# Optimization experiments

Hardware: AMD Instinct MI355X
Metric: run time of the kernel (lower is better)

Reference implementation:

```python
import jax, jax.numpy as jnp
import numpy as np
import math

D_MODEL = 1024
NUM_HEADS = 16
HEAD_DIM = D_MODEL // NUM_HEADS
CLAMP = 1e9


def setup_inputs() -> dict:
    key = jax.random.key(0)
    k1, k2, k3, k4, k5 = jax.random.split(key, 5)
    B, S = 2, 2048
    x = jax.random.normal(k1, (B, S, D_MODEL), dtype=jnp.float32)
    # torch Linear params, stored as [in, out] (y = x @ W + b)
    s1 = 1.0 / math.sqrt(D_MODEL)
    W_qkv = jax.random.uniform(k2, (D_MODEL, 3 * D_MODEL), jnp.float32, -s1, s1)
    b_qkv = jax.random.uniform(k3, (3 * D_MODEL,), jnp.float32, -s1, s1)
    W_out = jax.random.uniform(k4, (D_MODEL, D_MODEL), jnp.float32, -s1, s1)
    b_out = jax.random.uniform(k5, (D_MODEL,), jnp.float32, -s1, s1)
    return {"x": x, "W_qkv": W_qkv, "b_qkv": b_qkv, "W_out": W_out, "b_out": b_out}


def reference(x, W_qkv, b_qkv, W_out, b_out):
    B, S, D = x.shape
    qkv = x @ W_qkv + b_qkv                       # [B, S, 3*D]
    qkv = qkv.reshape(B, S, NUM_HEADS, 3 * HEAD_DIM).transpose(0, 2, 1, 3)  # [B, H, S, 3*hd]
    q, k, v = jnp.split(qkv, 3, axis=-1)          # each [B, H, S, hd]
    scale = 1.0 / math.sqrt(HEAD_DIM)
    scores = jnp.einsum('bhqd,bhkd->bhqk', q, k) * scale  # [B, H, S, S]
    causal = jnp.tril(jnp.ones((S, S), dtype=bool))
    scores = jnp.where(causal, scores, -jnp.inf)
    scores = jnp.clip(scores, -CLAMP, CLAMP)      # -inf -> -1e9, matching torch clamp
    attn = jax.nn.softmax(scores, axis=-1)
    values = jnp.einsum('bhqk,bhkd->bhqd', attn, v)        # [B, H, S, hd]
    values = values.transpose(0, 2, 1, 3).reshape(B, S, D)  # [B, S, D]
    out = values @ W_out + b_out
    # dropout is identity in eval mode
    return out
```

## Files before the change

kernel.cpp:

```cpp
#include <hip/hip_runtime.h>
#include <hip/hip_bf16.h>

#define D_MODEL 1024
#define NUM_HEADS 16
#define HEAD_DIM 64
#define SEQ 2048
#define BATCH 2
#define ROWS (BATCH * SEQ)

typedef unsigned short u16;
typedef __bf16 bf16x8 __attribute__((ext_vector_type(8)));
typedef float f32x4 __attribute__((ext_vector_type(4)));

__device__ inline u16 f2bfu(float f) {
  unsigned u = __float_as_uint(f);
  unsigned r = (u + 0x7fffu + ((u >> 16) & 1u)) >> 16;
  return (u16)r;
}

__device__ inline unsigned cvt_pk_bf16(float a, float b) {
#if __has_builtin(__builtin_amdgcn_cvt_pk_bf16_f32)
  auto r = __builtin_amdgcn_cvt_pk_bf16_f32(a, b);
  unsigned u;
  __builtin_memcpy(&u, &r, 4);
  return u;
#else
  return (unsigned)f2bfu(a) | ((unsigned)f2bfu(b) << 16);
#endif
}

__device__ inline f32x4 mfma16(bf16x8 a, bf16x8 b, f32x4 c) {
  return __builtin_amdgcn_mfma_f32_16x16x32_bf16(a, b, c, 0, 0, 0);
}

__device__ inline bf16x8 load_frag(const u16* p) {
  union { uint4 v; bf16x8 f; } u;
  u.v = *(const uint4*)p;
  return u.f;
}

__device__ inline void gload_lds16(const u16* g, u16* l) {
  __builtin_amdgcn_global_load_lds((const __attribute__((address_space(1))) void*)g,
                                   (__attribute__((address_space(3))) void*)l, 16, 0, 0);
}


__global__ __launch_bounds__(256) void prep_kernel(const float* __restrict__ x,
                                                   u16* __restrict__ xb,
                                                   const float* __restrict__ Wq,
                                                   u16* __restrict__ WqT,
                                                   const float* __restrict__ Wo,
                                                   u16* __restrict__ WoT) {
  __shared__ float t[32][33];
  const int bid = blockIdx.x;
  if (bid < 4096) {
    int i = bid * 256 + threadIdx.x;
    float4 v = ((const float4*)x)[i];
    uint2 o;
    o.x = cvt_pk_bf16(v.x, v.y);
    o.y = cvt_pk_bf16(v.z, v.w);
    ((uint2*)xb)[i] = o;
    return;
  }
  const float* W;
  u16* Wt;
  int N, tIdx;
  if (bid < 4096 + 3072) { W = Wq; Wt = WqT; N = 3072; tIdx = bid - 4096; }
  else                   { W = Wo; Wt = WoT; N = 1024; tIdx = bid - 7168; }
  const int k0 = (tIdx & 31) * 32, n0 = (tIdx >> 5) * 32;
  const int c = threadIdx.x & 31, r8 = threadIdx.x >> 5;
#pragma unroll
  for (int i = 0; i < 4; i++) {
    int r = r8 + i * 8;
    t[r][c] = W[(size_t)(k0 + r) * N + n0 + c];
  }
  __syncthreads();
#pragma unroll
  for (int i = 0; i < 4; i++) {
    int r = r8 + i * 8;
    Wt[(size_t)(n0 + r) * 1024 + k0 + c] = f2bfu(t[c][r]);
  }
}


__global__ __launch_bounds__(256, 3) void gemm_qkv(const u16* __restrict__ A,
                                                   const u16* __restrict__ Bt,
                                                   const float* __restrict__ bias,
                                                   u16* __restrict__ Qb, u16* __restrict__ Kb,
                                                   u16* __restrict__ Vt) {
  __shared__ u16 lA[3][128 * 32], lB[3][128 * 32];
  const int tid = threadIdx.x;
  const int wave = tid >> 6, lane = tid & 63, ln = lane & 15, quad = lane >> 4;
  const int lin = blockIdx.y * 24 + blockIdx.x;
  const int reg = lin & 7, idx = lin >> 3;
  const int mr = idx / 12, nr = idx - mr * 12;
  const int m0 = ((reg >> 1) * 8 + mr) * 128;
  const int n0 = (((reg & 1) * 12) + nr) * 128;
  const int wm = (wave & 1) * 64, wn = (wave >> 1) * 64;
  f32x4 acc[4][4] = {};

  auto issue = [&](u16* dA, u16* dB, int k0) {
#pragma unroll
    for (int i = 0; i < 2; ++i) {
      int rb = wave * 2 + i;
      gload_lds16(A + (size_t)(m0 + rb * 16 + ln) * 1024 + k0 + quad * 8, dA + rb * 512);
      gload_lds16(Bt + (size_t)(n0 + rb * 16 + ln) * 1024 + k0 + quad * 8, dB + rb * 512);
    }
  };
  auto compute = [&](const u16* sA, const u16* sB) {
    bf16x8 a[4], b[4];
#pragma unroll
    for (int i = 0; i < 4; ++i) {
      a[i] = load_frag(sA + (wm / 16 + i) * 512 + quad * 128 + ln * 8);
      b[i] = load_frag(sB + (wn / 16 + i) * 512 + quad * 128 + ln * 8);
    }
#pragma unroll
    for (int mt = 0; mt < 4; ++mt)
#pragma unroll
      for (int nt = 0; nt < 4; ++nt) acc[mt][nt] = mfma16(a[mt], b[nt], acc[mt][nt]);
  };

  issue(lA[0], lB[0], 0);
  issue(lA[1], lB[1], 32);
  asm volatile("s_waitcnt vmcnt(4)" ::: "memory");
  asm volatile("s_barrier" ::: "memory");

  for (int tt = 0; tt < 10; ++tt) {
    const int t = tt * 3;
    issue(lA[2], lB[2], (t + 2) * 32);
    compute(lA[0], lB[0]);
    asm volatile("s_waitcnt vmcnt(4)" ::: "memory");
    asm volatile("s_barrier" ::: "memory");
    issue(lA[0], lB[0], (t + 3) * 32);
    compute(lA[1], lB[1]);
    asm volatile("s_waitcnt vmcnt(4)" ::: "memory");
    asm volatile("s_barrier" ::: "memory");
    issue(lA[1], lB[1], (t + 4) * 32);
    compute(lA[2], lB[2]);
    asm volatile("s_waitcnt vmcnt(4)" ::: "memory");
    asm volatile("s_barrier" ::: "memory");
  }
  compute(lA[0], lB[0]);
  asm volatile("s_waitcnt vmcnt(0)" ::: "memory");
  asm volatile("s_barrier" ::: "memory");
  compute(lA[1], lB[1]);

#pragma unroll
  for (int mt = 0; mt < 4; ++mt) {
    int row = m0 + wm + mt * 16 + quad * 4;
    int bb = row >> 11, s0 = row & 2047;
#pragma unroll
    for (int nt = 0; nt < 4; ++nt) {
      int col = n0 + wn + nt * 16 + ln;
      float bv = bias[col];
      int h = col / 192, rem = col - h * 192, t3 = rem >> 6, d = rem & 63;
      int bh = bb * NUM_HEADS + h;
      if (t3 == 2) {
        uint2 pk;
        pk.x = cvt_pk_bf16(acc[mt][nt][0] + bv, acc[mt][nt][1] + bv);
        pk.y = cvt_pk_bf16(acc[mt][nt][2] + bv, acc[mt][nt][3] + bv);
        *(uint2*)(Vt + ((size_t)bh * 64 + d) * SEQ + s0) = pk;
      } else {
        u16* dst = (t3 == 0) ? Qb : Kb;
#pragma unroll
        for (int r = 0; r < 4; ++r)
          dst[((size_t)bh * SEQ + s0 + r) * 64 + d] = f2bfu(acc[mt][nt][r] + bv);
      }
    }
  }
}


__global__ __launch_bounds__(512) void attn_kernel(const u16* __restrict__ Qb,
                                                   const u16* __restrict__ Kb,
                                                   const u16* __restrict__ Vt,
                                                   u16* __restrict__ Ob) {
  __shared__ u16 lK[2 * 2 * 64 * 64];
  __shared__ u16 lV[2 * 64 * 64];
  __shared__ u16 lP[8][1152];
  const int tid = threadIdx.x;
  const int wave = tid >> 6, lane = tid & 63;
  const int ln = lane & 15, quad = lane >> 4;
  const int lin = blockIdx.y * 16 + blockIdx.x;
  const int xreg = lin & 7, xidx = lin >> 3;
  const int j = xidx & 15;
  const int bh = xreg * 4 + (xidx >> 4);
  const int lo = j, hi = 31 - j;
  const int myt = (wave < 4) ? lo : hi;
  const int q0w = myt * 64 + (wave & 3) * 16;
  const int sD = myt >> 1;
  const int nsup = (hi + 2) >> 1;
  const u16* Qg = Qb + (size_t)bh * SEQ * 64;
  const u16* Kg = Kb + (size_t)bh * SEQ * 64;
  const u16* Vg = Vt + (size_t)bh * 64 * SEQ;
  u16* lPw = lP[wave];

  bf16x8 qf[2];
#pragma unroll
  for (int ks = 0; ks < 2; ++ks)
    qf[ks] = load_frag(Qg + (size_t)(q0w + ln) * 64 + ks * 32 + quad * 8);

  const u16* sp[4];
  u16* dp[4];
#pragma unroll
  for (int i = 0; i < 4; ++i) {
    if (wave < 4) {
      int c = wave * 4 + i, half = c >> 3, cc = c & 7, rb = cc >> 1, kgh = cc & 1;
      sp[i] = Kg + (size_t)(half * 64 + rb * 16 + ln) * 64 + (kgh * 4 + quad) * 8;
      dp[i] = lK + half * 4096 + rb * 1024 + kgh * 512;
    } else {
      int c2 = wave * 4 - 16 + i, half = c2 >> 3, cc = c2 & 7, rb = cc >> 1, kgh = cc & 1;
      sp[i] = Vg + (size_t)(rb * 16 + ln) * SEQ + half * 64 + (kgh * 4 + quad) * 8;
      dp[i] = lV + half * 4096 + rb * 1024 + kgh * 512;
    }
  }
  if (wave < 4) {
#pragma unroll
    for (int i = 0; i < 4; ++i) gload_lds16(sp[i], dp[i]);
  }

  f32x4 o[4] = {};
  float m_r = -1e30f;
  float l_r = 0.f;
  const float SC = 0.18033688011112042f;
  const int qq = q0w + ln;

  for (int s = 0; s < nsup; ++s) {
    __syncthreads();
    if (wave >= 4) {
#pragma unroll
      for (int i = 0; i < 4; ++i) gload_lds16(sp[i] + (size_t)s * 128, dp[i]);
    }

    if (s <= sD) {
      const u16* lKs = lK + (s & 1) * 8192;
      f32x4 sc[2][4] = {};
#pragma unroll
      for (int h = 0; h < 2; ++h)
#pragma unroll
        for (int mt = 0; mt < 4; ++mt)
#pragma unroll
          for (int ks = 0; ks < 2; ++ks) {
            bf16x8 kf = load_frag(lKs + h * 4096 + mt * 1024 + (ks * 4 + quad) * 128 + ln * 8);
            sc[h][mt] = mfma16(kf, qf[ks], sc[h][mt]);
          }
      if (s == sD) {
#pragma unroll
        for (int h = 0; h < 2; ++h)
#pragma unroll
          for (int mt = 0; mt < 4; ++mt) {
            int key0 = (2 * s + h) * 64 + mt * 16 + quad * 4;
#pragma unroll
            for (int r = 0; r < 4; ++r)
              if (key0 + r > qq) sc[h][mt][r] = -1e30f;
          }
      }
      float mloc = sc[0][0][0];
#pragma unroll
      for (int h = 0; h < 2; ++h)
#pragma unroll
        for (int mt = 0; mt < 4; ++mt)
#pragma unroll
          for (int r = 0; r < 4; ++r) mloc = fmaxf(mloc, sc[h][mt][r]);
      mloc = fmaxf(mloc, __shfl_xor(mloc, 16));
      mloc = fmaxf(mloc, __shfl_xor(mloc, 32));
      float mnew = fmaxf(m_r, mloc);
      float alpha = __builtin_amdgcn_exp2f((m_r - mnew) * SC);
      float nmsc = -mnew * SC;
      float sum = 0.f;
#pragma unroll
      for (int h = 0; h < 2; ++h)
#pragma unroll
        for (int mt = 0; mt < 4; ++mt)
#pragma unroll
          for (int r = 0; r < 4; ++r) {
            float p = __builtin_amdgcn_exp2f(__builtin_fmaf(sc[h][mt][r], SC, nmsc));
            sc[h][mt][r] = p;
            sum += p;
          }
      sum += __shfl_xor(sum, 16);
      sum += __shfl_xor(sum, 32);
      l_r = l_r * alpha + sum;
      m_r = mnew;
#pragma unroll
      for (int dt = 0; dt < 4; ++dt) o[dt] *= alpha;

      __syncthreads();
      if (wave < 4 && s + 1 < nsup) {
        u16* dsl = (u16*)((s + 1) & 1 ? 8192 : 0);
#pragma unroll
        for (int i = 0; i < 4; ++i)
          gload_lds16(sp[i] + (size_t)(s + 1) * (128 * 64), dp[i] + ((s + 1) & 1) * 8192);
        (void)dsl;
      }

#pragma unroll
      for (int h = 0; h < 2; ++h) {
#pragma unroll
        for (int mt = 0; mt < 4; ++mt) {
          uint2 pk;
          pk.x = cvt_pk_bf16(sc[h][mt][0], sc[h][mt][1]);
          pk.y = cvt_pk_bf16(sc[h][mt][2], sc[h][mt][3]);
          int addr = ln * 64 + (((mt * 2 + (quad >> 1)) ^ (ln & 7)) * 8) + (quad & 1) * 4;
          *(uint2*)(lPw + addr) = pk;
        }
        bf16x8 pf[2];
#pragma unroll
        for (int ks = 0; ks < 2; ++ks)
          pf[ks] = load_frag(lPw + ln * 64 + (((ks * 4 + quad) ^ (ln & 7)) * 8));
#pragma unroll
        for (int dt = 0; dt < 4; ++dt)
#pragma unroll
          for (int ks = 0; ks < 2; ++ks) {
            bf16x8 av = load_frag(lV + h * 4096 + dt * 1024 + (ks * 4 + quad) * 128 + ln * 8);
            o[dt] = mfma16(av, pf[ks], o[dt]);
          }
      }
    } else {
      __syncthreads();
      if (wave < 4 && s + 1 < nsup) {
#pragma unroll
        for (int i = 0; i < 4; ++i)
          gload_lds16(sp[i] + (size_t)(s + 1) * (128 * 64), dp[i] + ((s + 1) & 1) * 8192);
      }
    }
  }

  float inv = 1.f / l_r;
#pragma unroll
  for (int dt = 0; dt < 4; ++dt) {
    uint2 pk;
    pk.x = cvt_pk_bf16(o[dt][0] * inv, o[dt][1] * inv);
    pk.y = cvt_pk_bf16(o[dt][2] * inv, o[dt][3] * inv);
    *(uint2*)(lPw + ln * 72 + dt * 16 + quad * 4) = pk;
  }
  const int b = bh >> 4, h2 = bh & 15;
#pragma unroll
  for (int i = 0; i < 2; ++i) {
    int c = lane + i * 64;
    int qq2 = c >> 3, dg = c & 7;
    uint4 val = *(const uint4*)(lPw + qq2 * 72 + dg * 8);
    *(uint4*)(Ob + ((size_t)b * SEQ + q0w + qq2) * 1024 + h2 * 64 + dg * 8) = val;
  }
}


__global__ __launch_bounds__(256, 3) void gemm_out(const u16* __restrict__ A,
                                                   const u16* __restrict__ Bt,
                                                   const float* __restrict__ bias,
                                                   float* __restrict__ out) {
  __shared__ u16 lA[3][128 * 32], lB[3][64 * 32];
  const int tid = threadIdx.x;
  const int wave = tid >> 6, lane = tid & 63, ln = lane & 15, quad = lane >> 4;
  const int lin = blockIdx.y * 16 + blockIdx.x;
  const int reg = lin & 7, idx = lin >> 3;
  const int mr = idx >> 3, nr = idx & 7;
  const int m0 = ((reg >> 1) * 8 + mr) * 128;
  const int n0 = (((reg & 1) * 8) + nr) * 64;
  f32x4 acc[2][4] = {};

  auto issue = [&](u16* dA, u16* dB, int k0) {
#pragma unroll
    for (int i = 0; i < 3; ++i) {
      int c = wave * 3 + i;
      if (c < 8) {
        gload_lds16(A + (size_t)(m0 + c * 16 + ln) * 1024 + k0 + quad * 8, dA + c * 512);
      } else {
        int cc = c - 8;
        gload_lds16(Bt + (size_t)(n0 + cc * 16 + ln) * 1024 + k0 + quad * 8, dB + cc * 512);
      }
    }
  };
  auto compute = [&](const u16* sA, const u16* sB) {
    bf16x8 a[2], b[4];
#pragma unroll
    for (int i = 0; i < 2; ++i)
      a[i] = load_frag(sA + (wave * 2 + i) * 512 + quad * 128 + ln * 8);
#pragma unroll
    for (int i = 0; i < 4; ++i)
      b[i] = load_frag(sB + i * 512 + quad * 128 + ln * 8);
#pragma unroll
    for (int mt = 0; mt < 2; ++mt)
#pragma unroll
      for (int nt = 0; nt < 4; ++nt) acc[mt][nt] = mfma16(a[mt], b[nt], acc[mt][nt]);
  };

  issue(lA[0], lB[0], 0);
  issue(lA[1], lB[1], 32);
  asm volatile("s_waitcnt vmcnt(3)" ::: "memory");
  asm volatile("s_barrier" ::: "memory");

  for (int tt = 0; tt < 10; ++tt) {
    const int t = tt * 3;
    issue(lA[2], lB[2], (t + 2) * 32);
    compute(lA[0], lB[0]);
    asm volatile("s_waitcnt vmcnt(3)" ::: "memory");
    asm volatile("s_barrier" ::: "memory");
    issue(lA[0], lB[0], (t + 3) * 32);
    compute(lA[1], lB[1]);
    asm volatile("s_waitcnt vmcnt(3)" ::: "memory");
    asm volatile("s_barrier" ::: "memory");
    issue(lA[1], lB[1], (t + 4) * 32);
    compute(lA[2], lB[2]);
    asm volatile("s_waitcnt vmcnt(3)" ::: "memory");
    asm volatile("s_barrier" ::: "memory");
  }
  compute(lA[0], lB[0]);
  asm volatile("s_waitcnt vmcnt(0)" ::: "memory");
  asm volatile("s_barrier" ::: "memory");
  compute(lA[1], lB[1]);

#pragma unroll
  for (int mt = 0; mt < 2; ++mt) {
    int row = m0 + wave * 32 + mt * 16 + quad * 4;
#pragma unroll
    for (int nt = 0; nt < 4; ++nt) {
      int col = n0 + nt * 16 + ln;
      float bv = bias[col];
#pragma unroll
      for (int r = 0; r < 4; ++r)
        out[(size_t)(row + r) * 1024 + col] = acc[mt][nt][r] + bv;
    }
  }
}


extern "C" void kernel_launch(void* const* d_in, const int* in_sizes, int n_in,
                              void* d_out, int out_size, void* d_ws, size_t ws_size,
                              hipStream_t stream) {
  const float* x = (const float*)d_in[0];
  const float* W_qkv = (const float*)d_in[1];
  const float* b_qkv = (const float*)d_in[2];
  const float* W_out = (const float*)d_in[3];
  const float* b_out = (const float*)d_in[4];
  float* out = (float*)d_out;

  char* ws = (char*)d_ws;
  const size_t SZ_XB = (size_t)ROWS * D_MODEL * 2;
  const size_t SZ_WQKVT = (size_t)3 * D_MODEL * D_MODEL * 2;
  const size_t SZ_WOUTT = (size_t)D_MODEL * D_MODEL * 2;
  const size_t SZ_HEADS = (size_t)BATCH * NUM_HEADS * SEQ * HEAD_DIM * 2;
  u16* xb = (u16*)(ws);
  u16* WqkvT = (u16*)(ws + SZ_XB);
  u16* WoutT = (u16*)(ws + SZ_XB + SZ_WQKVT);
  u16* Qb = (u16*)(ws + SZ_XB + SZ_WQKVT + SZ_WOUTT);
  u16* Kb = (u16*)(ws + SZ_XB + SZ_WQKVT + SZ_WOUTT + SZ_HEADS);
  u16* Vt = (u16*)(ws + SZ_XB + SZ_WQKVT + SZ_WOUTT + 2 * SZ_HEADS);
  u16* Ob = (u16*)(ws + SZ_XB + SZ_WQKVT + SZ_WOUTT + 3 * SZ_HEADS);

  prep_kernel<<<dim3(8192), dim3(256), 0, stream>>>(x, xb, W_qkv, WqkvT, W_out, WoutT);
  gemm_qkv<<<dim3(3 * D_MODEL / 128, ROWS / 128), dim3(256), 0, stream>>>(xb, WqkvT, b_qkv,
                                                                          Qb, Kb, Vt);
  attn_kernel<<<dim3(SEQ / 128, BATCH * NUM_HEADS), dim3(512), 0, stream>>>(Qb, Kb, Vt, Ob);
  gemm_out<<<dim3(D_MODEL / 64, ROWS / 128), dim3(256), 0, stream>>>(Ob, WoutT, b_out, out);
}
```

Baseline: 202.2 us.

## Add MFMA priority hints, lazy softmax rescale, and deeper K tiles in output GEMM

In the attention kernel, the MFMA sections are wrapped in s_setprio so matrix work gets issue priority over other waves. The online-softmax max update becomes lazy: the running max, O and l are rescaled only when some lane's new max exceeds the old one by a threshold, which skips the per-tile exp and multiply work. The output GEMM doubles its K tile from 32 to 64 per stage and lowers the occupancy bound to 2 to make room for the larger LDS buffers. This cuts the number of barriers and pipeline steps, at the cost of occupancy and a slightly different numerical path in the softmax.

```diff
diff --git a/kernel.cpp b/kernel.cpp
--- a/kernel.cpp
+++ b/kernel.cpp
@@ -235,6 +235,7 @@
     if (s <= sD) {
       const u16* lKs = lK + (s & 1) * 8192;
       f32x4 sc[2][4] = {};
+      __builtin_amdgcn_s_setprio(1);
 #pragma unroll
       for (int h = 0; h < 2; ++h)
 #pragma unroll
@@ -244,6 +245,7 @@
             bf16x8 kf = load_frag(lKs + h * 4096 + mt * 1024 + (ks * 4 + quad) * 128 + ln * 8);
             sc[h][mt] = mfma16(kf, qf[ks], sc[h][mt]);
           }
+      __builtin_amdgcn_s_setprio(0);
       if (s == sD) {
 #pragma unroll
         for (int h = 0; h < 2; ++h)
@@ -264,9 +266,15 @@
           for (int r = 0; r < 4; ++r) mloc = fmaxf(mloc, sc[h][mt][r]);
       mloc = fmaxf(mloc, __shfl_xor(mloc, 16));
       mloc = fmaxf(mloc, __shfl_xor(mloc, 32));
-      float mnew = fmaxf(m_r, mloc);
-      float alpha = __builtin_amdgcn_exp2f((m_r - mnew) * SC);
-      float nmsc = -mnew * SC;
+      if (!__all(mloc - m_r <= 44.0f)) {
+        float mnew = fmaxf(m_r, mloc);
+        float alpha = __builtin_amdgcn_exp2f((m_r - mnew) * SC);
+        l_r *= alpha;
+#pragma unroll
+        for (int dt = 0; dt < 4; ++dt) o[dt] *= alpha;
+        m_r = mnew;
+      }
+      float nmsc = -m_r * SC;
       float sum = 0.f;
 #pragma unroll
       for (int h = 0; h < 2; ++h)
@@ -280,18 +288,13 @@
           }
       sum += __shfl_xor(sum, 16);
       sum += __shfl_xor(sum, 32);
-      l_r = l_r * alpha + sum;
-      m_r = mnew;
-#pragma unroll
-      for (int dt = 0; dt < 4; ++dt) o[dt] *= alpha;
+      l_r += sum;
 
       __syncthreads();
       if (wave < 4 && s + 1 < nsup) {
-        u16* dsl = (u16*)((s + 1) & 1 ? 8192 : 0);
 #pragma unroll
         for (int i = 0; i < 4; ++i)
           gload_lds16(sp[i] + (size_t)(s + 1) * (128 * 64), dp[i] + ((s + 1) & 1) * 8192);
-        (void)dsl;
       }
 
 #pragma unroll
@@ -308,6 +311,7 @@
 #pragma unroll
         for (int ks = 0; ks < 2; ++ks)
           pf[ks] = load_frag(lPw + ln * 64 + (((ks * 4 + quad) ^ (ln & 7)) * 8));
+        __builtin_amdgcn_s_setprio(1);
 #pragma unroll
         for (int dt = 0; dt < 4; ++dt)
 #pragma unroll
@@ -315,6 +319,7 @@
             bf16x8 av = load_frag(lV + h * 4096 + dt * 1024 + (ks * 4 + quad) * 128 + ln * 8);
             o[dt] = mfma16(av, pf[ks], o[dt]);
           }
+        __builtin_amdgcn_s_setprio(0);
       }
     } else {
       __syncthreads();
@@ -345,11 +350,11 @@
 }
 
 
-__global__ __launch_bounds__(256, 3) void gemm_out(const u16* __restrict__ A,
+__global__ __launch_bounds__(256, 2) void gemm_out(const u16* __restrict__ A,
                                                    const u16* __restrict__ Bt,
                                                    const float* __restrict__ bias,
                                                    float* __restrict__ out) {
-  __shared__ u16 lA[3][128 * 32], lB[3][64 * 32];
+  __shared__ u16 lA[3][128 * 64], lB[3][64 * 64];
   const int tid = threadIdx.x;
   const int wave = tid >> 6, lane = tid & 63, ln = lane & 15, quad = lane >> 4;
   const int lin = blockIdx.y * 16 + blockIdx.x;
@@ -361,54 +366,71 @@
 
   auto issue = [&](u16* dA, u16* dB, int k0) {
 #pragma unroll
-    for (int i = 0; i < 3; ++i) {
-      int c = wave * 3 + i;
-      if (c < 8) {
-        gload_lds16(A + (size_t)(m0 + c * 16 + ln) * 1024 + k0 + quad * 8, dA + c * 512);
+    for (int i = 0; i < 6; ++i) {
+      int c = wave * 6 + i;
+      if (c < 16) {
+        int kh = c & 1, rb = c >> 1;
+        gload_lds16(A + (size_t)(m0 + rb * 16 + ln) * 1024 + k0 + kh * 32 + quad * 8,
+                    dA + kh * 4096 + rb * 512);
       } else {
-        int cc = c - 8;
-        gload_lds16(Bt + (size_t)(n0 + cc * 16 + ln) * 1024 + k0 + quad * 8, dB + cc * 512);
+        int c2 = c - 16, kh = c2 & 1, rbn = c2 >> 1;
+        gload_lds16(Bt + (size_t)(n0 + rbn * 16 + ln) * 1024 + k0 + kh * 32 + quad * 8,
+                    dB + kh * 2048 + rbn * 512);
       }
     }
   };
   auto compute = [&](const u16* sA, const u16* sB) {
-    bf16x8 a[2], b[4];
-#pragma unroll
-    for (int i = 0; i < 2; ++i)
-      a[i] = load_frag(sA + (wave * 2 + i) * 512 + quad * 128 + ln * 8);
-#pragma unroll
-    for (int i = 0; i < 4; ++i)
-      b[i] = load_frag(sB + i * 512 + quad * 128 + ln * 8);
-#pragma unroll
-    for (int mt = 0; mt < 2; ++mt)
-#pragma unroll
-      for (int nt = 0; nt < 4; ++nt) acc[mt][nt] = mfma16(a[mt], b[nt], acc[mt][nt]);
+    bf16x8 a[2][2], b[4][2];
+#pragma unroll
+    for (int ks = 0; ks < 2; ++ks) {
+#pragma unroll
+      for (int i = 0; i < 2; ++i)
+        a[i][ks] = load_frag(sA + ks * 4096 + (wave * 2 + i) * 512 + quad * 128 + ln * 8);
+#pragma unroll
+      for (int i = 0; i < 4; ++i)
+        b[i][ks] = load_frag(sB + ks * 2048 + i * 512 + quad * 128 + ln * 8);
+    }
+#pragma unroll
+    for (int ks = 0; ks < 2; ++ks)
+#pragma unroll
+      for (int mt = 0; mt < 2; ++mt)
+#pragma unroll
+        for (int nt = 0; nt < 4; ++nt)
+          acc[mt][nt] = mfma16(a[mt][ks], b[nt][ks], acc[mt][nt]);
   };
 
   issue(lA[0], lB[0], 0);
-  issue(lA[1], lB[1], 32);
-  asm volatile("s_waitcnt vmcnt(3)" ::: "memory");
-  asm volatile("s_barrier" ::: "memory");
-
-  for (int tt = 0; tt < 10; ++tt) {
+  issue(lA[1], lB[1], 64);
+  asm volatile("s_waitcnt vmcnt(6)" ::: "memory");
+  asm volatile("s_barrier" ::: "memory");
+
+  for (int tt = 0; tt < 4; ++tt) {
     const int t = tt * 3;
-    issue(lA[2], lB[2], (t + 2) * 32);
+    issue(lA[2], lB[2], (t + 2) * 64);
     compute(lA[0], lB[0]);
-    asm volatile("s_waitcnt vmcnt(3)" ::: "memory");
-    asm volatile("s_barrier" ::: "memory");
-    issue(lA[0], lB[0], (t + 3) * 32);
+    asm volatile("s_waitcnt vmcnt(6)" ::: "memory");
+    asm volatile("s_barrier" ::: "memory");
+    issue(lA[0], lB[0], (t + 3) * 64);
     compute(lA[1], lB[1]);
-    asm volatile("s_waitcnt vmcnt(3)" ::: "memory");
-    asm volatile("s_barrier" ::: "memory");
-    issue(lA[1], lB[1], (t + 4) * 32);
+    asm volatile("s_waitcnt vmcnt(6)" ::: "memory");
+    asm volatile("s_barrier" ::: "memory");
+    issue(lA[1], lB[1], (t + 4) * 64);
     compute(lA[2], lB[2]);
-    asm volatile("s_waitcnt vmcnt(3)" ::: "memory");
-    asm volatile("s_barrier" ::: "memory");
-  }
+    asm volatile("s_waitcnt vmcnt(6)" ::: "memory");
+    asm volatile("s_barrier" ::: "memory");
+  }
+  issue(lA[2], lB[2], 14 * 64);
   compute(lA[0], lB[0]);
+  asm volatile("s_waitcnt vmcnt(6)" ::: "memory");
+  asm volatile("s_barrier" ::: "memory");
+  issue(lA[0], lB[0], 15 * 64);
+  compute(lA[1], lB[1]);
+  asm volatile("s_waitcnt vmcnt(6)" ::: "memory");
+  asm volatile("s_barrier" ::: "memory");
+  compute(lA[2], lB[2]);
   asm volatile("s_waitcnt vmcnt(0)" ::: "memory");
   asm volatile("s_barrier" ::: "memory");
-  compute(lA[1], lB[1]);
+  compute(lA[0], lB[0]);
 
 #pragma unroll
   for (int mt = 0; mt < 2; ++mt) {
```

Result: no change. 200.7 us (-0.7%).
